# Performance work log

Measured on AMD Instinct MI355X. Metric: run time of the kernel, lower is better.

## Reference

```python
import jax, jax.numpy as jnp
import numpy as np

V, E, T, H, Z = 32000, 512, 64, 1024, 128
B = 64
PAD = 31999


def _lin(x, W, b):
    return x @ W.T + b


def _lstm_cell(x, h, c, Wih, Whh, bih, bhh):
    gates = x @ Wih.T + bih + h @ Whh.T + bhh  # [B,4H], torch gate order i,f,g,o
    i, f, g, o = jnp.split(gates, 4, axis=-1)
    c = jax.nn.sigmoid(f) * c + jax.nn.sigmoid(i) * jnp.tanh(g)
    h = jax.nn.sigmoid(o) * jnp.tanh(c)
    return h, c


def _forward(enc_input, dec_input, length, eps, enc_emb, enc_Wih, enc_Whh, enc_bih, enc_bhh,
             latent_W, latent_b, dec_emb, attn_W, attn_b, combine_W, combine_b,
             dec_Wih, dec_Whh, dec_bih, dec_bhh, pri_W, pri_b, inf_W, inf_b,
             aux_W, aux_b, out_W, out_b):
    # All lengths == T, so the descending sort and pack/pad are identity ops.
    att_mask = enc_input == PAD  # [B,T]
    x_enc = enc_emb[enc_input]   # [B,T,E]

    def enc_step(carry, x):
        h, c = carry
        h, c = _lstm_cell(x, h, c, enc_Wih, enc_Whh, enc_bih, enc_bhh)
        return (h, c), h

    h0 = jnp.zeros((B, H), x_enc.dtype)
    (h_T, c_T), enc_out = jax.lax.scan(enc_step, (h0, h0), jnp.swapaxes(x_enc, 0, 1))
    enc_output = jnp.swapaxes(enc_out, 0, 1)  # [B,T,H]

    mu, logvar = jnp.split(_lin(jnp.concatenate([h_T, c_T], -1), latent_W, latent_b), 2, -1)
    z = mu + jnp.exp(0.5 * logvar) * eps  # [B,Z]

    x_dec = dec_emb[dec_input]  # [B,T+1,E]; dropout off (eval mode)

    def dec_step(carry, inp):
        h, c = carry
        x, t = inp
        pri_mu, pri_lv = jnp.split(_lin(h, pri_W, pri_b), 2, -1)
        scale = _lin(jnp.concatenate([x, h], -1), attn_W, attn_b)  # [B,T]
        scale = jnp.where(att_mask, -jnp.inf, scale)
        attn_w = jax.nn.softmax(scale, -1)
        context = jnp.einsum('bt,bth->bh', attn_w, enc_output)
        inf_mu, inf_lv = jnp.split(_lin(jnp.concatenate([h, context], -1), inf_W, inf_b), 2, -1)
        mask = (length + 1 > t).astype(x.dtype)  # [B]
        kld = 0.5 * jnp.sum(pri_lv - inf_lv + jnp.exp(inf_lv - pri_lv)
                            + (inf_mu - pri_mu) ** 2 / jnp.exp(pri_lv) - 1.0, axis=1) * mask
        z_step = pri_mu  # eval mode (torch: reparameterize(inf_mu, inf_lv) when training)
        aux_mu = _lin(z_step, aux_W, aux_b)
        aux_c = jnp.sum((jax.lax.stop_gradient(context) - aux_mu) ** 2, axis=1)
        u = _lin(jnp.concatenate([x, aux_mu, z_step, z], -1), combine_W, combine_b)
        h, c = _lstm_cell(u, h, c, dec_Wih, dec_Whh, dec_bih, dec_bhh)
        return (h, c), (h, kld, aux_c)

    ts = jnp.arange(T + 1)
    _, (hs, klds, aux_cs) = jax.lax.scan(dec_step, (h0, h0), (jnp.swapaxes(x_dec, 0, 1), ts))
    output = jnp.swapaxes(hs, 0, 1)  # [B,T+1,H]

    logit = output @ out_W.T + out_b  # [B,T+1,V]
    logp = jax.nn.log_softmax(logit, -1)
    return logp, mu, logvar, jnp.sum(klds), jnp.sum(aux_cs)


def setup_inputs() -> dict:
    key = jax.random.key(0)
    ks = jax.random.split(key, 32)
    s = 0.02
    d = {
        'enc_input': jax.random.randint(ks[0], (B, T), 0, V - 1),
        'dec_input': jax.random.randint(ks[1], (B, T + 1), 0, V - 1),
        'length': jnp.full((B,), T, dtype=jnp.int32),
        'eps': jax.random.normal(ks[2], (B, Z), jnp.float32),
        'enc_emb': (jax.random.normal(ks[3], (V, E)) * s).at[PAD].set(0.0),
        'enc_Wih': jax.random.normal(ks[4], (4 * H, E)) * s,
        'enc_Whh': jax.random.normal(ks[5], (4 * H, H)) * s,
        'enc_bih': jax.random.normal(ks[6], (4 * H,)) * s,
        'enc_bhh': jax.random.normal(ks[7], (4 * H,)) * s,
        'latent_W': jax.random.normal(ks[8], (2 * Z, 2 * H)) * s,
        'latent_b': jax.random.normal(ks[9], (2 * Z,)) * s,
        'dec_emb': (jax.random.normal(ks[10], (V, E)) * s).at[PAD].set(0.0),
        'attn_W': jax.random.normal(ks[11], (T, H + E)) * s,
        'attn_b': jax.random.normal(ks[12], (T,)) * s,
        'combine_W': jax.random.normal(ks[13], (H, H + E + 2 * Z)) * s,
        'combine_b': jax.random.normal(ks[14], (H,)) * s,
        'dec_Wih': jax.random.normal(ks[15], (4 * H, H)) * s,
        'dec_Whh': jax.random.normal(ks[16], (4 * H, H)) * s,
        'dec_bih': jax.random.normal(ks[17], (4 * H,)) * s,
        'dec_bhh': jax.random.normal(ks[18], (4 * H,)) * s,
        'pri_W': jax.random.normal(ks[19], (2 * Z, H)) * s,
        'pri_b': jax.random.normal(ks[20], (2 * Z,)) * s,
        'inf_W': jax.random.normal(ks[21], (2 * Z, 2 * H)) * s,
        'inf_b': jax.random.normal(ks[22], (2 * Z,)) * s,
        'aux_W': jax.random.normal(ks[23], (H, Z)) * s,
        'aux_b': jax.random.normal(ks[24], (H,)) * s,
        'out_W': jax.random.normal(ks[25], (V, H)) * s,
        'out_b': jax.random.normal(ks[26], (V,)) * s,
    }
    return d


def reference(enc_input, dec_input, length, eps, enc_emb, enc_Wih, enc_Whh, enc_bih, enc_bhh,
              latent_W, latent_b, dec_emb, attn_W, attn_b, combine_W, combine_b,
              dec_Wih, dec_Whh, dec_bih, dec_bhh, pri_W, pri_b, inf_W, inf_b,
              aux_W, aux_b, out_W, out_b):
    return _forward(enc_input, dec_input, length, eps, enc_emb, enc_Wih, enc_Whh, enc_bih,
                    enc_bhh, latent_W, latent_b, dec_emb, attn_W, attn_b, combine_W, combine_b,
                    dec_Wih, dec_Whh, dec_bih, dec_bhh, pri_W, pri_b, inf_W, inf_b,
                    aux_W, aux_b, out_W, out_b)
```

## Files before the change

### kernel.cpp

```cpp
#include <hip/hip_runtime.h>
#include <hip/hip_bf16.h>
#include <cmath>

typedef unsigned short u16;
typedef __attribute__((ext_vector_type(8))) short short8;
typedef __attribute__((ext_vector_type(4))) float floatx4;

#define DEVI __device__ __forceinline__

constexpr int cV = 32000, cE = 512, cT = 64, cH = 1024, cZ = 128, cB = 64, cPAD = 31999, cTP1 = 65;
constexpr long long LOGP_SZ = 133120000LL;
constexpr long long AMAT_OFF = 130990080LL;
constexpr long long WBOUT_OFF = 38400000LL;
constexpr int SKIP_LO = 1200, SKIP_HI = 1712;

DEVI float b2f(u16 u) { return __uint_as_float(((unsigned)u) << 16); }
DEVI u16 f2b(float f) {
  unsigned u = __float_as_uint(f);
  unsigned r = u + 0x7FFFu + ((u >> 16) & 1u);
  return (u16)(r >> 16);
}
DEVI unsigned pk2(float lo, float hi) {
  __hip_bfloat162 t = __float22bfloat162_rn(make_float2(lo, hi));
  return *reinterpret_cast<unsigned*>(&t);
}
DEVI float sigm(float x) { return 1.f / (1.f + expf(-x)); }

DEVI short8 ldfragW(const float* __restrict__ p) {
  float4 x = *(const float4*)p, y = *(const float4*)(p + 4);
  union { unsigned u[4]; short8 s; } r;
  r.u[0] = pk2(x.x, x.y); r.u[1] = pk2(x.z, x.w);
  r.u[2] = pk2(y.x, y.y); r.u[3] = pk2(y.z, y.w);
  return r.s;
}

template <typename T>
DEVI short8 ldfrag(const T* __restrict__ p) {
  if constexpr (sizeof(T) == 2) return *(const short8*)(p);
  else return ldfragW((const float*)p);
}

template <int MAP>
DEVI int rmap(int r) {
  if constexpr (MAP == 1) return ((r & 3) << 10) | (r >> 2);
  else if constexpr (MAP == 2) return r & 63;
  else return r;
}

DEVI float dot_wf(const float* __restrict__ w, const float* __restrict__ s, int K) {
  float a0 = 0.f, a1 = 0.f, a2 = 0.f, a3 = 0.f;
#pragma unroll 4
  for (int k = 0; k < K; k += 8) {
    float4 p = *(const float4*)(w + k);
    float4 q = *(const float4*)(w + k + 4);
    a0 = fmaf(s[k + 0], p.x, a0); a1 = fmaf(s[k + 1], p.y, a1);
    a2 = fmaf(s[k + 2], p.z, a2); a3 = fmaf(s[k + 3], p.w, a3);
    a0 = fmaf(s[k + 4], q.x, a0); a1 = fmaf(s[k + 5], q.y, a1);
    a2 = fmaf(s[k + 6], q.z, a2); a3 = fmaf(s[k + 7], q.w, a3);
  }
  return (a0 + a1) + (a2 + a3);
}

__global__ __launch_bounds__(256) void k_zero(float* p, int n) {
  int i = blockIdx.x * 256 + threadIdx.x;
  if (i < n) p[i] = 0.f;
}

template <typename AT, typename BT, typename CT, int AMAP, int BMAP, bool ADDC>
__global__ __launch_bounds__(64) void k_gemm(
    const AT* __restrict__ A, int lda, const BT* __restrict__ B, int ldb,
    const float* __restrict__ bias, const float* __restrict__ Dm, int ldd,
    CT* __restrict__ C, int ldc, int K) {
  int nblk = blockIdx.x, mblk = blockIdx.y;
  int lane = threadIdx.x;
  int lr = lane & 15, kg = lane >> 4;
  const BT* Bp = B + (size_t)rmap<BMAP>(nblk * 16 + lr) * ldb + kg * 8;
  const AT* Ap[4];
#pragma unroll
  for (int mf = 0; mf < 4; mf++)
    Ap[mf] = A + (size_t)rmap<AMAP>(mblk * 64 + mf * 16 + lr) * lda + kg * 8;
  floatx4 acc[4];
#pragma unroll
  for (int mf = 0; mf < 4; mf++) acc[mf] = (floatx4){0.f, 0.f, 0.f, 0.f};
#pragma unroll 4
  for (int ks = 0; ks < K / 32; ks++) {
    short8 bv = ldfrag(Bp + ks * 32);
#pragma unroll
    for (int mf = 0; mf < 4; mf++) {
      short8 av = ldfrag(Ap[mf] + ks * 32);
      acc[mf] = __builtin_amdgcn_mfma_f32_16x16x32_bf16(av, bv, acc[mf], 0, 0, 0);
    }
  }
  int n = nblk * 16 + lr;
  float bs = bias ? bias[n] : 0.f;
#pragma unroll
  for (int mf = 0; mf < 4; mf++) {
#pragma unroll
    for (int jj = 0; jj < 4; jj++) {
      int m = mblk * 64 + mf * 16 + kg * 4 + jj;
      size_t ci = (size_t)m * ldc + n;
      float v = acc[mf][jj] + bs;
      if (Dm) v += Dm[(size_t)rmap<AMAP>(m) * ldd + n];
      if constexpr (ADDC) {
        if constexpr (sizeof(CT) == 2) v += b2f(C[ci]);
        else v += C[ci];
      }
      if constexpr (sizeof(CT) == 2) C[ci] = f2b(v);
      else C[ci] = v;
    }
  }
}

__global__ __launch_bounds__(64) void k_cell2(
    const u16* __restrict__ G, const u16* __restrict__ H, int strideH,
    const u16* __restrict__ Wb, float* __restrict__ c,
    u16* __restrict__ out1, int s1, u16* __restrict__ Afrag, int t) {
  int nb = blockIdx.x;
  int lane = threadIdx.x;
  int lr = lane & 15, kg = lane >> 4;
  const u16* Bp = Wb + (size_t)(nb * 16 + lr) * cH + kg * 8;
  floatx4 acc[4];
#pragma unroll
  for (int mf = 0; mf < 4; mf++) acc[mf] = (floatx4){0.f, 0.f, 0.f, 0.f};
#pragma unroll 8
  for (int ks = 0; ks < 32; ks++) {
    short8 bv = *(const short8*)(Bp + ks * 32);
#pragma unroll
    for (int mf = 0; mf < 4; mf++) {
      short8 av = *(const short8*)(H + (size_t)(mf * 16 + lr) * strideH + ks * 32 + kg * 8);
      acc[mf] = __builtin_amdgcn_mfma_f32_16x16x32_bf16(av, bv, acc[mf], 0, 0, 0);
    }
  }
  __shared__ float lds[16][65];
#pragma unroll
  for (int mf = 0; mf < 4; mf++)
#pragma unroll
    for (int jj = 0; jj < 4; jj++)
      lds[lr][mf * 16 + kg * 4 + jj] = acc[mf][jj];
  __syncthreads();
#pragma unroll
  for (int a = 0; a < 4; a++) {
    int b = lane;
    int j = nb * 4 + a;
    ushort4 gv = *(const ushort4*)(G + (size_t)b * 4096 + nb * 16 + 4 * a);
    float gi = lds[4 * a + 0][b] + b2f(gv.x);
    float gf = lds[4 * a + 1][b] + b2f(gv.y);
    float gg = lds[4 * a + 2][b] + b2f(gv.z);
    float go = lds[4 * a + 3][b] + b2f(gv.w);
    int ci = b * cH + j;
    float cc = c[ci];
    cc = sigm(gf) * cc + sigm(gi) * tanhf(gg);
    float hh = sigm(go) * tanhf(cc);
    c[ci] = cc;
    u16 hb = f2b(hh);
    out1[(size_t)b * s1 + j] = hb;
    if (Afrag) {
      int m = b * cTP1 + t;
      size_t idx = ((size_t)(m >> 4) * 32 + (j >> 5)) * 512 +
                   ((((j >> 3) & 3) * 16) + (m & 15)) * 8 + (j & 7);
      Afrag[idx] = hb;
    }
  }
}

__global__ __launch_bounds__(256) void k_tr(const float* __restrict__ src, int ld,
                                            int R, float* __restrict__ dst) {
  __shared__ float tile[32][33];
  int c0 = blockIdx.x * 32, r0 = blockIdx.y * 32;
  int tx = threadIdx.x & 31, ty = threadIdx.x >> 5;
  for (int i = ty; i < 32; i += 8) tile[i][tx] = src[(size_t)(r0 + i) * ld + c0 + tx];
  __syncthreads();
  for (int i = ty; i < 32; i += 8) dst[(size_t)(c0 + i) * R + r0 + tx] = tile[tx][i];
}

__global__ __launch_bounds__(256) void k_gemv(const float* __restrict__ W, int ld,
                                              const float* __restrict__ x,
                                              const float* __restrict__ b,
                                              float* __restrict__ out, int K, int add) {
  int n = blockIdx.x * 256 + threadIdx.x;
  const float* w = W + (size_t)n * ld;
  float s = b ? b[n] : 0.f;
  for (int k = 0; k < K; k += 4) {
    float4 wv = *(const float4*)(w + k);
    float4 xv = *(const float4*)(x + k);
    s += wv.x * xv.x + wv.y * xv.y + wv.z * xv.z + wv.w * xv.w;
  }
  if (add) out[n] += s; else out[n] = s;
}

__global__ __launch_bounds__(256) void k_biasD(const float* __restrict__ bih,
                                               const float* __restrict__ bhh,
                                               const float* __restrict__ Wih,
                                               const float* __restrict__ u0,
                                               float* __restrict__ biasD) {
  int np = blockIdx.x * 256 + threadIdx.x;
  int src = ((np & 3) << 10) | (np >> 2);
  const float* w = Wih + (size_t)src * cH;
  float s = bih[src] + bhh[src];
  for (int k = 0; k < cH; k += 4) {
    float4 wv = *(const float4*)(w + k);
    float4 xv = *(const float4*)(u0 + k);
    s += wv.x * xv.x + wv.y * xv.y + wv.z * xv.z + wv.w * xv.w;
  }
  biasD[np] = s;
}

__global__ __launch_bounds__(256) void k_biasE(const float* __restrict__ bih,
                                               const float* __restrict__ bhh,
                                               float* __restrict__ biasE) {
  int np = blockIdx.x * 256 + threadIdx.x;
  int src = ((np & 3) << 10) | (np >> 2);
  biasE[np] = bih[src] + bhh[src];
}

__global__ __launch_bounds__(256) void k_permW(const float* __restrict__ Whh,
                                               u16* __restrict__ Wp) {
  int np = blockIdx.x;
  int src = ((np & 3) << 10) | (np >> 2);
  const float* w = Whh + (size_t)src * cH;
  u16* d = Wp + (size_t)np * cH;
  int tid = threadIdx.x;
#pragma unroll
  for (int p = 0; p < 4; p++) d[tid + p * 256] = f2b(w[tid + p * 256]);
}

__global__ __launch_bounds__(256) void k_cvtW(const float* __restrict__ W,
                                              u16* __restrict__ Wf) {
  int g = blockIdx.x * 4 + (threadIdx.x >> 6);
  int l = threadIdx.x & 63;
  int nblk = g >> 5, kb = g & 31;
  const float* src = W + (size_t)(nblk * 16 + (l & 15)) * cH + kb * 32 + (l >> 4) * 8;
  *(short8*)(Wf + (size_t)g * 512 + l * 8) = ldfragW(src);
}

__global__ __launch_bounds__(256) void k_gather(const int* __restrict__ tok,
                                                const float* __restrict__ emb,
                                                u16* __restrict__ dst, int Tlen) {
  int r = blockIdx.x;
  int t = r >> 6, b = r & 63;
  const float* src = emb + (size_t)tok[b * Tlen + t] * cE;
  u16* d = dst + (size_t)r * cE;
  int tid = threadIdx.x;
  for (int k = tid; k < cE; k += 256) d[k] = f2b(src[k]);
}

__global__ __launch_bounds__(256) void k_latent(
    const u16* __restrict__ encO, const float* __restrict__ cT2,
    const float* __restrict__ W, const float* __restrict__ bias,
    float* __restrict__ mulv, float* __restrict__ outp) {
  __shared__ float s[2 * cH];
  int b = blockIdx.x;
  int n = threadIdx.x;
  for (int k = n; k < cH; k += 256) {
    s[k] = b2f(encO[((size_t)b * cT + 63) * cH + k]);
    s[cH + k] = cT2[b * cH + k];
  }
  __syncthreads();
  float acc = bias[n] + dot_wf(W + (size_t)n * (2 * cH), s, 2 * cH);
  mulv[b * 256 + n] = acc;
  if (n < cZ)
    outp[LOGP_SZ + (size_t)b * cZ + n] = acc;
  else
    outp[LOGP_SZ + (size_t)cB * cZ + (size_t)b * cZ + (n - cZ)] = acc;
}

__global__ __launch_bounds__(256) void k_z(const float* __restrict__ mulv,
                                           const float* __restrict__ eps,
                                           u16* __restrict__ zbuf) {
  int i = blockIdx.x * 256 + threadIdx.x;
  if (i >= cB * cZ) return;
  int b = i >> 7, zi = i & 127;
  float mu = mulv[b * 256 + zi], lv = mulv[b * 256 + cZ + zi];
  zbuf[i] = f2b(mu + expf(0.5f * lv) * eps[i]);
}

__global__ __launch_bounds__(256) void k_sctx(
    const float* __restrict__ S, const int* __restrict__ enc_input,
    const u16* __restrict__ encO, u16* __restrict__ ctxH) {
  __shared__ float wat[cT];
  int tb = blockIdx.x;
  int b = tb & 63;
  int tid = threadIdx.x;
  if (tid < cT) {
    float sc = S[(size_t)tb * cT + tid];
    if (enc_input[b * cT + tid] == cPAD) sc = -INFINITY;
    float m = sc;
#pragma unroll
    for (int off = 32; off >= 1; off >>= 1) m = fmaxf(m, __shfl_xor(m, off));
    float p = expf(sc - m);
    float ssum = p;
#pragma unroll
    for (int off = 32; off >= 1; off >>= 1) ssum += __shfl_xor(ssum, off);
    wat[tid] = p / ssum;
  }
  __syncthreads();
#pragma unroll
  for (int p = 0; p < 4; p++) {
    int j = tid + p * 256;
    float s = 0.f;
    const u16* e = encO + ((size_t)b * cT) * cH + j;
#pragma unroll 8
    for (int t2 = 0; t2 < cT; t2++) s += wat[t2] * b2f(e[(size_t)t2 * cH]);
    ctxH[(size_t)tb * cH + j] = f2b(s);
  }
}

__global__ __launch_bounds__(256) void k_scal_all(
    const float* __restrict__ priH, const float* __restrict__ infH,
    const u16* __restrict__ ctxH, const u16* __restrict__ auxH,
    const int* __restrict__ length, float* __restrict__ scal) {
  __shared__ float red[256];
  int tb = blockIdx.x;
  int t = tb >> 6, b = tb & 63;
  int tid = threadIdx.x;
  float r = 0.f;
  if (tid < cZ) {
    float pm = priH[(size_t)tb * 256 + tid], plv = priH[(size_t)tb * 256 + cZ + tid];
    float im = infH[(size_t)tb * 256 + tid], ilv = infH[(size_t)tb * 256 + cZ + tid];
    float d = im - pm;
    r = plv - ilv + expf(ilv - plv) + d * d * expf(-plv) - 1.f;
  }
  red[tid] = r;
  __syncthreads();
  for (int sft = 128; sft > 0; sft >>= 1) {
    if (tid < sft) red[tid] += red[tid + sft];
    __syncthreads();
  }
  if (tid == 0 && (length[b] + 1 > t)) atomicAdd(&scal[0], 0.5f * red[0]);
  __syncthreads();
  float r2 = 0.f;
#pragma unroll
  for (int p = 0; p < 4; p++) {
    int j = tid + p * 256;
    float d = b2f(ctxH[(size_t)tb * cH + j]) - b2f(auxH[(size_t)tb * cH + j]);
    r2 += d * d;
  }
  red[tid] = r2;
  __syncthreads();
  for (int sft = 128; sft > 0; sft >>= 1) {
    if (tid < sft) red[tid] += red[tid + sft];
    __syncthreads();
  }
  if (tid == 0) atomicAdd(&scal[1], red[0]);
}

__global__ void k_scal(const float* __restrict__ scal, float* __restrict__ outp) {
  if (threadIdx.x == 0) {
    outp[LOGP_SZ + 2 * cB * cZ] = scal[0];
    outp[LOGP_SZ + 2 * cB * cZ + 1] = scal[1];
  }
}

__global__ __launch_bounds__(256) void k_cpyA(const u16* __restrict__ src,
                                              u16* __restrict__ dst) {
  int i = blockIdx.x * 256 + threadIdx.x;
  ((uint4*)dst)[i] = ((const uint4*)(src + (size_t)252 * 32 * 512))[i];
}

template <bool WFRAG>
__global__ __launch_bounds__(512) void k_logit3(
    const u16* __restrict__ Af, int fragBase,
    const u16* __restrict__ Wf, const float* __restrict__ Wraw,
    const float* __restrict__ bias, float* __restrict__ outp,
    int mStart, int mEnd, int storeLo, int storeHi, int skipLo, int skipHi) {
  __shared__ u16 wpan[32768];
  int nb = blockIdx.x;
  int tid = threadIdx.x;
  if constexpr (WFRAG) {
    const uint4* src = (const uint4*)(Wf + (size_t)nb * 32768);
    uint4* dst = (uint4*)wpan;
#pragma unroll
    for (int q = 0; q < 8; q++) dst[tid + q * 512] = src[tid + q * 512];
  } else {
    int wv = tid >> 6, l = tid & 63;
    for (int f = wv; f < 64; f += 8) {
      int fr = f >> 5, kb = f & 31;
      const float* src = Wraw + (size_t)(nb * 32 + fr * 16 + (l & 15)) * cH + kb * 32 + (l >> 4) * 8;
      *(short8*)(wpan + f * 512 + l * 8) = ldfragW(src);
    }
  }
  __syncthreads();
  int wave = tid >> 6, lane = tid & 63;
  int lr = lane & 15, kg = lane >> 4;
  for (int m0 = mStart; m0 < mEnd; m0 += 512) {
    int mi = m0 + wave * 64;
    int mfg[4];
#pragma unroll
    for (int mf = 0; mf < 4; mf++) {
      int g = (mi >> 4) + mf;
      if (g > 259) g = 259;
      mfg[mf] = g - fragBase;
    }
    floatx4 acc[4][2];
#pragma unroll
    for (int mf = 0; mf < 4; mf++)
#pragma unroll
      for (int ni = 0; ni < 2; ni++) acc[mf][ni] = (floatx4){0.f, 0.f, 0.f, 0.f};
#pragma unroll 4
    for (int ks = 0; ks < 32; ks++) {
      short8 bv0 = *(const short8*)(wpan + ks * 512 + lane * 8);
      short8 bv1 = *(const short8*)(wpan + (32 + ks) * 512 + lane * 8);
#pragma unroll
      for (int mf = 0; mf < 4; mf++) {
        short8 av = *(const short8*)(Af + ((size_t)mfg[mf] * 32 + ks) * 512 + lane * 8);
        acc[mf][0] = __builtin_amdgcn_mfma_f32_16x16x32_bf16(av, bv0, acc[mf][0], 0, 0, 0);
        acc[mf][1] = __builtin_amdgcn_mfma_f32_16x16x32_bf16(av, bv1, acc[mf][1], 0, 0, 0);
      }
    }
#pragma unroll
    for (int mf = 0; mf < 4; mf++) {
#pragma unroll
      for (int ni = 0; ni < 2; ni++) {
        int n = nb * 32 + ni * 16 + lr;
        float bb = bias[n];
#pragma unroll
        for (int jj = 0; jj < 4; jj++) {
          int m = mi + mf * 16 + kg * 4 + jj;
          if (m >= storeLo && m < storeHi && !(m >= skipLo && m < skipHi))
            outp[(size_t)m * cV + n] = acc[mf][ni][jj] + bb;
        }
      }
    }
  }
}

__global__ __launch_bounds__(256) void k_lsm(float* __restrict__ outp) {
  __shared__ float wm_[4], ws_[4];
  __shared__ float blz;
  int m = blockIdx.x;
  int tid = threadIdx.x, lane = tid & 63, wid = tid >> 6;
  float4* rp4 = (float4*)(outp + (size_t)m * cV);
  float mx = -INFINITY, sm = 0.f;
  for (int n = tid; n < cV / 4; n += 256) {
    float4 v = rp4[n];
    float lm = fmaxf(fmaxf(v.x, v.y), fmaxf(v.z, v.w));
    float nm = fmaxf(mx, lm);
    sm = sm * expf(mx - nm) + expf(v.x - nm) + expf(v.y - nm) + expf(v.z - nm) + expf(v.w - nm);
    mx = nm;
  }
#pragma unroll
  for (int off = 32; off >= 1; off >>= 1) {
    float om = __shfl_xor(mx, off), os = __shfl_xor(sm, off);
    float nm = fmaxf(mx, om);
    sm = sm * expf(mx - nm) + os * expf(om - nm);
    mx = nm;
  }
  if (lane == 0) { wm_[wid] = mx; ws_[wid] = sm; }
  __syncthreads();
  if (tid == 0) {
    float M = fmaxf(fmaxf(wm_[0], wm_[1]), fmaxf(wm_[2], wm_[3]));
    float S = ws_[0] * expf(wm_[0] - M) + ws_[1] * expf(wm_[1] - M) +
              ws_[2] * expf(wm_[2] - M) + ws_[3] * expf(wm_[3] - M);
    blz = M + logf(S);
  }
  __syncthreads();
  float lz = blz;
  for (int n = tid; n < cV / 4; n += 256) {
    float4 v = rp4[n];
    v.x -= lz; v.y -= lz; v.z -= lz; v.w -= lz;
    rp4[n] = v;
  }
}

extern "C" void kernel_launch(void* const* d_in, const int* in_sizes, int n_in,
                              void* d_out, int out_size, void* d_ws, size_t ws_size,
                              hipStream_t stream) {
  (void)in_sizes; (void)n_in; (void)out_size; (void)ws_size;
  const int* enc_input  = (const int*)d_in[0];
  const int* dec_input  = (const int*)d_in[1];
  const int* length     = (const int*)d_in[2];
  const float* eps      = (const float*)d_in[3];
  const float* enc_emb  = (const float*)d_in[4];
  const float* enc_Wih  = (const float*)d_in[5];
  const float* enc_Whh  = (const float*)d_in[6];
  const float* enc_bih  = (const float*)d_in[7];
  const float* enc_bhh  = (const float*)d_in[8];
  const float* latent_W = (const float*)d_in[9];
  const float* latent_b = (const float*)d_in[10];
  const float* dec_emb  = (const float*)d_in[11];
  const float* attn_W   = (const float*)d_in[12];
  const float* attn_b   = (const float*)d_in[13];
  const float* comb_W   = (const float*)d_in[14];
  const float* comb_b   = (const float*)d_in[15];
  const float* dec_Wih  = (const float*)d_in[16];
  const float* dec_Whh  = (const float*)d_in[17];
  const float* dec_bih  = (const float*)d_in[18];
  const float* dec_bhh  = (const float*)d_in[19];
  const float* pri_W    = (const float*)d_in[20];
  const float* pri_b    = (const float*)d_in[21];
  const float* inf_W    = (const float*)d_in[22];
  const float* inf_b    = (const float*)d_in[23];
  const float* aux_W    = (const float*)d_in[24];
  const float* aux_b    = (const float*)d_in[25];
  const float* out_W    = (const float*)d_in[26];
  const float* out_b    = (const float*)d_in[27];
  float* outp = (float*)d_out;
  float* outF = outp;

  size_t off = 0;
  float* c_enc = outF + off; off += 65536;
  float* c_dec = outF + off; off += 65536;
  float* scal  = outF + off; off += 4;
  off += 60;
  u16* HencZ = (u16*)(outF + off); off += 32768;
  u16* Hh    = (u16*)(outF + off); off += 66 * 32768;
  size_t zeroSpan = 196672;
  u16* encO  = (u16*)(outF + off); off += 2097152;
  u16* Xenc  = (u16*)(outF + off); off += 1048576;
  u16* Xdec  = (u16*)(outF + off); off += 1064960;
  u16* zbuf  = (u16*)(outF + off); off += 4096;
  float* mulv  = outF + off; off += 16384;
  float* biasE = outF + off; off += 4096;
  float* biasD = outF + off; off += 4096;
  float* tmp1  = outF + off; off += 1024;
  float* u0    = outF + off; off += 1024;
  float* WcxT  = outF + off; off += 524288;
  float* WczT  = outF + off; off += 131072;
  float* wPmT  = outF + off; off += 131072;
  float* auxWT = outF + off; off += 131072;
  float* M1    = outF + off; off += 131072;
  float* WfT   = outF + off; off += 1048576;
  u16* WhhEp = (u16*)(outF + off); off += 2097152;
  u16* Wbig  = (u16*)(outF + off); off += 2097152;
  u16* C1    = (u16*)(outF + off); off += 1048576;
  u16* C2    = (u16*)(outF + off); off += 262144;
  u16* Genc  = (u16*)(outF + off); off += 8388608;
  u16* Gdec  = (u16*)(outF + off); off += 8519680;
  float* priH = outF + off; off += 1064960;
  float* infH = outF + off; off += 1064960;
  float* S    = outF + off; off += 266240;
  u16* ctxH  = (u16*)(outF + off); off += 2129920;
  u16* auxH  = (u16*)(outF + off); off += 2129920;
  u16* Wf   = (u16*)(outF + WBOUT_OFF);
  u16* Amat = (u16*)(outF + AMAT_OFF);
  u16* wsA = (u16*)d_ws;

  k_cvtW<<<16000, 256, 0, stream>>>(out_W, Wf);
  k_tr<<<dim3(16, 32), 256, 0, stream>>>(comb_W, 1792, 1024, WcxT);
  k_tr<<<dim3(4, 32), 256, 0, stream>>>(comb_W + 1664, 1792, 1024, WczT);
  k_tr<<<dim3(32, 4), 256, 0, stream>>>(pri_W, 1024, 128, wPmT);
  k_tr<<<dim3(4, 32), 256, 0, stream>>>(aux_W, 128, 1024, auxWT);
  k_gemv<<<4, 256, 0, stream>>>(aux_W, 128, pri_b, aux_b, tmp1, 128, 0);
  k_gemv<<<4, 256, 0, stream>>>(comb_W + 512, 1792, tmp1, comb_b, u0, 1024, 0);
  k_gemv<<<4, 256, 0, stream>>>(comb_W + 1536, 1792, pri_b, nullptr, u0, 128, 1);
  k_biasE<<<16, 256, 0, stream>>>(enc_bih, enc_bhh, biasE);
  k_biasD<<<16, 256, 0, stream>>>(dec_bih, dec_bhh, dec_Wih, u0, biasD);
  k_permW<<<4096, 256, 0, stream>>>(enc_Whh, WhhEp);
  k_gather<<<cT * cB, 256, 0, stream>>>(enc_input, enc_emb, Xenc, cT);
  k_gather<<<cTP1 * cB, 256, 0, stream>>>(dec_input, dec_emb, Xdec, cTP1);
  k_zero<<<(int)((zeroSpan + 255) / 256), 256, 0, stream>>>(c_enc, (int)zeroSpan);

  k_gemm<float, float, float, 0, 0, false><<<dim3(8, 16), 64, 0, stream>>>(
      comb_W + 512, 1792, auxWT, 1024, nullptr, comb_W + 1536, 1792, M1, 128, 1024);
  k_gemm<float, float, float, 0, 0, false><<<dim3(64, 16), 64, 0, stream>>>(
      wPmT, 128, M1, 128, nullptr, nullptr, 0, WfT, 1024, 128);
  k_gemm<float, float, u16, 1, 0, false><<<dim3(64, 64), 64, 0, stream>>>(
      dec_Wih, 1024, WfT, 1024, nullptr, dec_Whh, 1024, Wbig, 1024, 1024);
  k_gemm<float, float, u16, 1, 0, false><<<dim3(32, 64), 64, 0, stream>>>(
      dec_Wih, 1024, WcxT, 1024, nullptr, nullptr, 0, C1, 512, 1024);
  k_gemm<float, float, u16, 1, 0, false><<<dim3(8, 64), 64, 0, stream>>>(
      dec_Wih, 1024, WczT, 1024, nullptr, nullptr, 0, C2, 128, 1024);
  k_gemm<u16, float, u16, 0, 1, false><<<dim3(256, 64), 64, 0, stream>>>(
      Xenc, 512, enc_Wih, 512, biasE, nullptr, 0, Genc, 4096, 512);

  for (int t = 0; t < cT; t++) {
    const u16* Hcur = t ? (encO + (size_t)(t - 1) * cH) : HencZ;
    int sH = t ? (cT * cH) : cH;
    k_cell2<<<256, 64, 0, stream>>>(Genc + (size_t)t * cB * 4096, Hcur, sH, WhhEp,
                                    c_enc, encO + (size_t)t * cH, cT * cH, nullptr, 0);
  }
  k_latent<<<cB, 256, 0, stream>>>(encO, c_enc, latent_W, latent_b, mulv, outp);
  k_z<<<(cB * cZ + 255) / 256, 256, 0, stream>>>(mulv, eps, zbuf);

  k_gemm<u16, u16, u16, 0, 0, false><<<dim3(256, 65), 64, 0, stream>>>(
      Xdec, 512, C1, 512, biasD, nullptr, 0, Gdec, 4096, 512);
  k_gemm<u16, u16, u16, 2, 0, true><<<dim3(256, 65), 64, 0, stream>>>(
      zbuf, 128, C2, 128, nullptr, nullptr, 0, Gdec, 4096, 128);

  for (int t = 0; t < cTP1; t++) {
    k_cell2<<<256, 64, 0, stream>>>(Gdec + (size_t)t * cB * 4096,
                                    Hh + (size_t)t * cB * cH, cH, Wbig, c_dec,
                                    Hh + (size_t)(t + 1) * cB * cH, cH,
                                    Amat, t);
  }

  k_gemm<u16, float, float, 0, 0, false><<<dim3(16, 65), 64, 0, stream>>>(
      Hh, 1024, pri_W, 1024, pri_b, nullptr, 0, priH, 256, 1024);
  k_gemm<u16, float, float, 0, 0, false><<<dim3(4, 65), 64, 0, stream>>>(
      Xdec, 512, attn_W, 1536, attn_b, nullptr, 0, S, 64, 512);
  k_gemm<u16, float, float, 0, 0, true><<<dim3(4, 65), 64, 0, stream>>>(
      Hh, 1024, attn_W + 512, 1536, nullptr, nullptr, 0, S, 64, 1024);
  k_sctx<<<cTP1 * cB, 256, 0, stream>>>(S, enc_input, encO, ctxH);
  k_gemm<u16, float, float, 0, 0, false><<<dim3(16, 65), 64, 0, stream>>>(
      Hh, 1024, inf_W, 2048, inf_b, nullptr, 0, infH, 256, 1024);
  k_gemm<u16, float, float, 0, 0, true><<<dim3(16, 65), 64, 0, stream>>>(
      ctxH, 1024, inf_W + 1024, 2048, nullptr, nullptr, 0, infH, 256, 1024);
  k_gemm<float, float, u16, 0, 0, false><<<dim3(64, 65), 64, 0, stream>>>(
      priH, 256, aux_W, 128, aux_b, nullptr, 0, auxH, 1024, 128);
  k_scal_all<<<cTP1 * cB, 256, 0, stream>>>(priH, infH, ctxH, auxH, length, scal);
  k_scal<<<1, 64, 0, stream>>>(scal, outp);

  k_cpyA<<<32, 256, 0, stream>>>(Amat, wsA);
  k_logit3<true><<<1000, 512, 0, stream>>>(Amat, 0, Wf, nullptr, out_b, outp,
                                           0, 4096, 0, 4093, SKIP_LO, SKIP_HI);
  k_logit3<false><<<1000, 512, 0, stream>>>(Amat, 0, nullptr, out_W, out_b, outp,
                                            SKIP_LO, SKIP_HI, SKIP_LO, SKIP_HI, 0, 0);
  k_logit3<false><<<1000, 512, 0, stream>>>(wsA, 252, nullptr, out_W, out_b, outp,
                                            4032, 4160, 4093, 4160, 0, 0);
  k_lsm<<<cB * cTP1, 256, 0, stream>>>(outp);
}
```

Before: 4.017 ms.

## Use fragment-packed weights and hidden state in LSTM steps, widen logit tiles

Pre-packs the encoder/decoder recurrent weights and input-projection weights into MFMA fragment order, so the GEMMs and the per-step cell kernel load contiguous short8 fragments instead of strided rows. The cell kernel now ping-pongs a fragment-layout hidden state and writes its outputs with vectorized ushort4/float4 stores. The logit kernel moves from 32 to 64 vocab columns per block with K split into two halves staged through the same LDS panel, halving the block count and reusing each A fragment across four B tiles. This adds workspace buffers and extra sync points in the logit kernel, and it relies on the shifted skip/offset constants staying consistent.

```diff
diff --git a/kernel.cpp b/kernel.cpp
--- a/kernel.cpp
+++ b/kernel.cpp
@@ -11,8 +11,8 @@
 constexpr int cV = 32000, cE = 512, cT = 64, cH = 1024, cZ = 128, cB = 64, cPAD = 31999, cTP1 = 65;
 constexpr long long LOGP_SZ = 133120000LL;
 constexpr long long AMAT_OFF = 130990080LL;
-constexpr long long WBOUT_OFF = 38400000LL;
-constexpr int SKIP_LO = 1200, SKIP_HI = 1712;
+constexpr long long WBOUT_OFF = 39936000LL;
+constexpr int SKIP_LO = 1248, SKIP_HI = 1760;
 
 DEVI float b2f(u16 u) { return __uint_as_float(((unsigned)u) << 16); }
 DEVI u16 f2b(float f) {
@@ -66,7 +66,8 @@
   if (i < n) p[i] = 0.f;
 }
 
-template <typename AT, typename BT, typename CT, int AMAP, int BMAP, bool ADDC>
+template <typename AT, typename BT, typename CT, int AMAP, int BMAP, bool ADDC,
+          int BFRAGKB = 0, bool CFRAG = false>
 __global__ __launch_bounds__(64) void k_gemm(
     const AT* __restrict__ A, int lda, const BT* __restrict__ B, int ldb,
     const float* __restrict__ bias, const float* __restrict__ Dm, int ldd,
@@ -84,7 +85,11 @@
   for (int mf = 0; mf < 4; mf++) acc[mf] = (floatx4){0.f, 0.f, 0.f, 0.f};
 #pragma unroll 4
   for (int ks = 0; ks < K / 32; ks++) {
-    short8 bv = ldfrag(Bp + ks * 32);
+    short8 bv;
+    if constexpr (BFRAGKB > 0)
+      bv = *(const short8*)((const u16*)B + ((size_t)nblk * BFRAGKB + ks) * 512 + lane * 8);
+    else
+      bv = ldfrag(Bp + ks * 32);
 #pragma unroll
     for (int mf = 0; mf < 4; mf++) {
       short8 av = ldfrag(Ap[mf] + ks * 32);
@@ -98,36 +103,45 @@
 #pragma unroll
     for (int jj = 0; jj < 4; jj++) {
       int m = mblk * 64 + mf * 16 + kg * 4 + jj;
-      size_t ci = (size_t)m * ldc + n;
       float v = acc[mf][jj] + bs;
       if (Dm) v += Dm[(size_t)rmap<AMAP>(m) * ldd + n];
-      if constexpr (ADDC) {
-        if constexpr (sizeof(CT) == 2) v += b2f(C[ci]);
-        else v += C[ci];
+      if constexpr (CFRAG) {
+        size_t fi = ((size_t)(m >> 4) * (ldc >> 5) + (n >> 5)) * 512 +
+                    (size_t)((((n >> 3) & 3) * 16 + (m & 15)) * 8 + (n & 7));
+        ((u16*)C)[fi] = f2b(v);
+      } else {
+        size_t ci = (size_t)m * ldc + n;
+        if constexpr (ADDC) {
+          if constexpr (sizeof(CT) == 2) v += b2f(C[ci]);
+          else v += C[ci];
+        }
+        if constexpr (sizeof(CT) == 2) C[ci] = f2b(v);
+        else C[ci] = v;
       }
-      if constexpr (sizeof(CT) == 2) C[ci] = f2b(v);
-      else C[ci] = v;
     }
   }
 }
 
-__global__ __launch_bounds__(64) void k_cell2(
-    const u16* __restrict__ G, const u16* __restrict__ H, int strideH,
-    const u16* __restrict__ Wb, float* __restrict__ c,
-    u16* __restrict__ out1, int s1, u16* __restrict__ Afrag, int t) {
+__global__ __launch_bounds__(64) void k_cell3(
+    const u16* __restrict__ G,
+    const u16* __restrict__ Hf,
+    const u16* __restrict__ Wbf,
+    float* __restrict__ c,
+    u16* __restrict__ outRM, int s1,
+    u16* __restrict__ HfOut,
+    u16* __restrict__ Afrag, int t) {
   int nb = blockIdx.x;
   int lane = threadIdx.x;
   int lr = lane & 15, kg = lane >> 4;
-  const u16* Bp = Wb + (size_t)(nb * 16 + lr) * cH + kg * 8;
   floatx4 acc[4];
 #pragma unroll
   for (int mf = 0; mf < 4; mf++) acc[mf] = (floatx4){0.f, 0.f, 0.f, 0.f};
 #pragma unroll 8
   for (int ks = 0; ks < 32; ks++) {
-    short8 bv = *(const short8*)(Bp + ks * 32);
+    short8 bv = *(const short8*)(Wbf + ((size_t)nb * 32 + ks) * 512 + lane * 8);
 #pragma unroll
     for (int mf = 0; mf < 4; mf++) {
-      short8 av = *(const short8*)(H + (size_t)(mf * 16 + lr) * strideH + ks * 32 + kg * 8);
+      short8 av = *(const short8*)(Hf + ((size_t)mf * 32 + ks) * 512 + lane * 8);
       acc[mf] = __builtin_amdgcn_mfma_f32_16x16x32_bf16(av, bv, acc[mf], 0, 0, 0);
     }
   }
@@ -138,28 +152,36 @@
     for (int jj = 0; jj < 4; jj++)
       lds[lr][mf * 16 + kg * 4 + jj] = acc[mf][jj];
   __syncthreads();
+  int b = lane;
+  const u16* gp = G + (size_t)b * 4096 + nb * 16;
+  float4 cc4 = *(const float4*)(c + (size_t)b * cH + nb * 4);
+  float cin[4] = {cc4.x, cc4.y, cc4.z, cc4.w};
+  float ncc[4];
+  u16 hb[4];
 #pragma unroll
   for (int a = 0; a < 4; a++) {
-    int b = lane;
-    int j = nb * 4 + a;
-    ushort4 gv = *(const ushort4*)(G + (size_t)b * 4096 + nb * 16 + 4 * a);
-    float gi = lds[4 * a + 0][b] + b2f(gv.x);
-    float gf = lds[4 * a + 1][b] + b2f(gv.y);
-    float gg = lds[4 * a + 2][b] + b2f(gv.z);
-    float go = lds[4 * a + 3][b] + b2f(gv.w);
-    int ci = b * cH + j;
-    float cc = c[ci];
+    float gi = lds[4 * a + 0][b] + b2f(gp[4 * a + 0]);
+    float gf = lds[4 * a + 1][b] + b2f(gp[4 * a + 1]);
+    float gg = lds[4 * a + 2][b] + b2f(gp[4 * a + 2]);
+    float go = lds[4 * a + 3][b] + b2f(gp[4 * a + 3]);
+    float cc = cin[a];
     cc = sigm(gf) * cc + sigm(gi) * tanhf(gg);
     float hh = sigm(go) * tanhf(cc);
-    c[ci] = cc;
-    u16 hb = f2b(hh);
-    out1[(size_t)b * s1 + j] = hb;
-    if (Afrag) {
-      int m = b * cTP1 + t;
-      size_t idx = ((size_t)(m >> 4) * 32 + (j >> 5)) * 512 +
-                   ((((j >> 3) & 3) * 16) + (m & 15)) * 8 + (j & 7);
-      Afrag[idx] = hb;
-    }
+    ncc[a] = cc;
+    hb[a] = f2b(hh);
+  }
+  *(float4*)(c + (size_t)b * cH + nb * 4) = make_float4(ncc[0], ncc[1], ncc[2], ncc[3]);
+  ushort4 hv = {hb[0], hb[1], hb[2], hb[3]};
+  *(ushort4*)(outRM + (size_t)b * s1 + nb * 4) = hv;
+  int j0 = nb * 4;
+  size_t hidx = ((size_t)(b >> 4) * 32 + (j0 >> 5)) * 512 +
+                (size_t)((((j0 >> 3) & 3) * 16 + (b & 15)) * 8 + (j0 & 7));
+  *(ushort4*)(HfOut + hidx) = hv;
+  if (Afrag) {
+    int m = b * cTP1 + t;
+    size_t aidx = ((size_t)(m >> 4) * 32 + (j0 >> 5)) * 512 +
+                  (size_t)((((j0 >> 3) & 3) * 16 + (m & 15)) * 8 + (j0 & 7));
+    *(ushort4*)(Afrag + aidx) = hv;
   }
 }
 
@@ -213,15 +235,16 @@
   biasE[np] = bih[src] + bhh[src];
 }
 
-__global__ __launch_bounds__(256) void k_permW(const float* __restrict__ Whh,
-                                               u16* __restrict__ Wp) {
-  int np = blockIdx.x;
+__global__ __launch_bounds__(256) void k_packP(const float* __restrict__ W,
+                                               u16* __restrict__ Wf, int K) {
+  int g = blockIdx.x * 4 + (threadIdx.x >> 6);
+  int l = threadIdx.x & 63;
+  int KB = K >> 5;
+  int nblk = g / KB, kb = g % KB;
+  int np = nblk * 16 + (l & 15);
   int src = ((np & 3) << 10) | (np >> 2);
-  const float* w = Whh + (size_t)src * cH;
-  u16* d = Wp + (size_t)np * cH;
-  int tid = threadIdx.x;
-#pragma unroll
-  for (int p = 0; p < 4; p++) d[tid + p * 256] = f2b(w[tid + p * 256]);
+  const float* s = W + (size_t)src * K + kb * 32 + (l >> 4) * 8;
+  *(short8*)(Wf + (size_t)g * 512 + l * 8) = ldfragW(s);
 }
 
 __global__ __launch_bounds__(256) void k_cvtW(const float* __restrict__ W,
@@ -358,7 +381,7 @@
 }
 
 template <bool WFRAG>
-__global__ __launch_bounds__(512) void k_logit3(
+__global__ __launch_bounds__(512) void k_logit4(
     const u16* __restrict__ Af, int fragBase,
     const u16* __restrict__ Wf, const float* __restrict__ Wraw,
     const float* __restrict__ bias, float* __restrict__ outp,
@@ -366,20 +389,6 @@
   __shared__ u16 wpan[32768];
   int nb = blockIdx.x;
   int tid = threadIdx.x;
-  if constexpr (WFRAG) {
-    const uint4* src = (const uint4*)(Wf + (size_t)nb * 32768);
-    uint4* dst = (uint4*)wpan;
-#pragma unroll
-    for (int q = 0; q < 8; q++) dst[tid + q * 512] = src[tid + q * 512];
-  } else {
-    int wv = tid >> 6, l = tid & 63;
-    for (int f = wv; f < 64; f += 8) {
-      int fr = f >> 5, kb = f & 31;
-      const float* src = Wraw + (size_t)(nb * 32 + fr * 16 + (l & 15)) * cH + kb * 32 + (l >> 4) * 8;
-      *(short8*)(wpan + f * 512 + l * 8) = ldfragW(src);
-    }
-  }
-  __syncthreads();
   int wave = tid >> 6, lane = tid & 63;
   int lr = lane & 15, kg = lane >> 4;
   for (int m0 = mStart; m0 < mEnd; m0 += 512) {
@@ -391,33 +400,57 @@
       if (g > 259) g = 259;
       mfg[mf] = g - fragBase;
     }
-    floatx4 acc[4][2];
+    floatx4 acc[4][4];
 #pragma unroll
     for (int mf = 0; mf < 4; mf++)
 #pragma unroll
-      for (int ni = 0; ni < 2; ni++) acc[mf][ni] = (floatx4){0.f, 0.f, 0.f, 0.f};
+      for (int fr = 0; fr < 4; fr++) acc[mf][fr] = (floatx4){0.f, 0.f, 0.f, 0.f};
+    for (int h = 0; h < 2; h++) {
+      __syncthreads();
+      if constexpr (WFRAG) {
+#pragma unroll
+        for (int q = 0; q < 8; q++) {
+          int idx = q * 4096 + tid * 8;
+          int lf = idx >> 9, wi = idx & 511;
+          int fr = lf >> 4, kbl = lf & 15;
+          size_t g = (size_t)(nb * 4 + fr) * 32 + h * 16 + kbl;
+          *(uint4*)(wpan + idx) = *(const uint4*)(Wf + g * 512 + wi);
+        }
+      } else {
+        for (int f = wave; f < 64; f += 8) {
+          int fr = f >> 4, kbl = f & 15;
+          const float* src = Wraw + (size_t)(nb * 64 + fr * 16 + lr) * cH +
+                             h * 512 + kbl * 32 + kg * 8;
+          *(short8*)(wpan + (size_t)f * 512 + lane * 8) = ldfragW(src);
+        }
+      }
+      __syncthreads();
 #pragma unroll 4
-    for (int ks = 0; ks < 32; ks++) {
-      short8 bv0 = *(const short8*)(wpan + ks * 512 + lane * 8);
-      short8 bv1 = *(const short8*)(wpan + (32 + ks) * 512 + lane * 8);
-#pragma unroll
-      for (int mf = 0; mf < 4; mf++) {
-        short8 av = *(const short8*)(Af + ((size_t)mfg[mf] * 32 + ks) * 512 + lane * 8);
-        acc[mf][0] = __builtin_amdgcn_mfma_f32_16x16x32_bf16(av, bv0, acc[mf][0], 0, 0, 0);
-        acc[mf][1] = __builtin_amdgcn_mfma_f32_16x16x32_bf16(av, bv1, acc[mf][1], 0, 0, 0);
+      for (int ks = 0; ks < 16; ks++) {
+        short8 bv[4];
+#pragma unroll
+        for (int fr = 0; fr < 4; fr++)
+          bv[fr] = *(const short8*)(wpan + ((size_t)(fr * 16 + ks) * 512) + lane * 8);
+#pragma unroll
+        for (int mf = 0; mf < 4; mf++) {
+          short8 av = *(const short8*)(Af + ((size_t)mfg[mf] * 32 + h * 16 + ks) * 512 + lane * 8);
+#pragma unroll
+          for (int fr = 0; fr < 4; fr++)
+            acc[mf][fr] = __builtin_amdgcn_mfma_f32_16x16x32_bf16(av, bv[fr], acc[mf][fr], 0, 0, 0);
+        }
       }
     }
 #pragma unroll
     for (int mf = 0; mf < 4; mf++) {
 #pragma unroll
-      for (int ni = 0; ni < 2; ni++) {
-        int n = nb * 32 + ni * 16 + lr;
+      for (int fr = 0; fr < 4; fr++) {
+        int n = nb * 64 + fr * 16 + lr;
         float bb = bias[n];
 #pragma unroll
         for (int jj = 0; jj < 4; jj++) {
           int m = mi + mf * 16 + kg * 4 + jj;
           if (m >= storeLo && m < storeHi && !(m >= skipLo && m < skipHi))
-            outp[(size_t)m * cV + n] = acc[mf][ni][jj] + bb;
+            outp[(size_t)m * cV + n] = acc[mf][fr][jj] + bb;
         }
       }
     }
@@ -502,9 +535,12 @@
   float* c_dec = outF + off; off += 65536;
   float* scal  = outF + off; off += 4;
   off += 60;
-  u16* HencZ = (u16*)(outF + off); off += 32768;
-  u16* Hh    = (u16*)(outF + off); off += 66 * 32768;
-  size_t zeroSpan = 196672;
+  u16* HfEncA = (u16*)(outF + off); off += 32768;
+  u16* HfDecA = (u16*)(outF + off); off += 32768;
+  u16* Hh     = (u16*)(outF + off); off += 66 * 32768;
+  size_t zeroSpan = 229440;
+  u16* HfEncB = (u16*)(outF + off); off += 32768;
+  u16* HfDecB = (u16*)(outF + off); off += 32768;
   u16* encO  = (u16*)(outF + off); off += 2097152;
   u16* Xenc  = (u16*)(outF + off); off += 1048576;
   u16* Xdec  = (u16*)(outF + off); off += 1064960;
@@ -520,10 +556,11 @@
   float* auxWT = outF + off; off += 131072;
   float* M1    = outF + off; off += 131072;
   float* WfT   = outF + off; off += 1048576;
-  u16* WhhEp = (u16*)(outF + off); off += 2097152;
-  u16* Wbig  = (u16*)(outF + off); off += 2097152;
-  u16* C1    = (u16*)(outF + off); off += 1048576;
-  u16* C2    = (u16*)(outF + off); off += 262144;
+  u16* WhhEpF = (u16*)(outF + off); off += 2097152;
+  u16* WbigF  = (u16*)(outF + off); off += 2097152;
+  u16* C1f    = (u16*)(outF + off); off += 1048576;
+  u16* C2f    = (u16*)(outF + off); off += 262144;
+  u16* WihEf  = (u16*)(outF + off); off += 1048576;
   u16* Genc  = (u16*)(outF + off); off += 8388608;
   u16* Gdec  = (u16*)(outF + off); off += 8519680;
   float* priH = outF + off; off += 1064960;
@@ -545,7 +582,8 @@
   k_gemv<<<4, 256, 0, stream>>>(comb_W + 1536, 1792, pri_b, nullptr, u0, 128, 1);
   k_biasE<<<16, 256, 0, stream>>>(enc_bih, enc_bhh, biasE);
   k_biasD<<<16, 256, 0, stream>>>(dec_bih, dec_bhh, dec_Wih, u0, biasD);
-  k_permW<<<4096, 256, 0, stream>>>(enc_Whh, WhhEp);
+  k_packP<<<2048, 256, 0, stream>>>(enc_Whh, WhhEpF, 1024);
+  k_packP<<<1024, 256, 0, stream>>>(enc_Wih, WihEf, 512);
   k_gather<<<cT * cB, 256, 0, stream>>>(enc_input, enc_emb, Xenc, cT);
   k_gather<<<cTP1 * cB, 256, 0, stream>>>(dec_input, dec_emb, Xdec, cTP1);
   k_zero<<<(int)((zeroSpan + 255) / 256), 256, 0, stream>>>(c_enc, (int)zeroSpan);
@@ -554,34 +592,36 @@
       comb_W + 512, 1792, auxWT, 1024, nullptr, comb_W + 1536, 1792, M1, 128, 1024);
   k_gemm<float, float, float, 0, 0, false><<<dim3(64, 16), 64, 0, stream>>>(
       wPmT, 128, M1, 128, nullptr, nullptr, 0, WfT, 1024, 128);
-  k_gemm<float, float, u16, 1, 0, false><<<dim3(64, 64), 64, 0, stream>>>(
-      dec_Wih, 1024, WfT, 1024, nullptr, dec_Whh, 1024, Wbig, 1024, 1024);
-  k_gemm<float, float, u16, 1, 0, false><<<dim3(32, 64), 64, 0, stream>>>(
-      dec_Wih, 1024, WcxT, 1024, nullptr, nullptr, 0, C1, 512, 1024);
-  k_gemm<float, float, u16, 1, 0, false><<<dim3(8, 64), 64, 0, stream>>>(
-      dec_Wih, 1024, WczT, 1024, nullptr, nullptr, 0, C2, 128, 1024);
-  k_gemm<u16, float, u16, 0, 1, false><<<dim3(256, 64), 64, 0, stream>>>(
-      Xenc, 512, enc_Wih, 512, biasE, nullptr, 0, Genc, 4096, 512);
+  k_gemm<float, float, u16, 1, 0, false, 0, true><<<dim3(64, 64), 64, 0, stream>>>(
+      dec_Wih, 1024, WfT, 1024, nullptr, dec_Whh, 1024, WbigF, 1024, 1024);
+  k_gemm<float, float, u16, 1, 0, false, 0, true><<<dim3(32, 64), 64, 0, stream>>>(
+      dec_Wih, 1024, WcxT, 1024, nullptr, nullptr, 0, C1f, 512, 1024);
+  k_gemm<float, float, u16, 1, 0, false, 0, true><<<dim3(8, 64), 64, 0, stream>>>(
+      dec_Wih, 1024, WczT, 1024, nullptr, nullptr, 0, C2f, 128, 1024);
+  k_gemm<u16, u16, u16, 0, 0, false, 16, false><<<dim3(256, 64), 64, 0, stream>>>(
+      Xenc, 512, WihEf, 512, biasE, nullptr, 0, Genc, 4096, 512);
 
   for (int t = 0; t < cT; t++) {
-    const u16* Hcur = t ? (encO + (size_t)(t - 1) * cH) : HencZ;
-    int sH = t ? (cT * cH) : cH;
-    k_cell2<<<256, 64, 0, stream>>>(Genc + (size_t)t * cB * 4096, Hcur, sH, WhhEp,
-                                    c_enc, encO + (size_t)t * cH, cT * cH, nullptr, 0);
+    const u16* hin = (t & 1) ? HfEncB : HfEncA;
+    u16* hout = (t & 1) ? HfEncA : HfEncB;
+    k_cell3<<<256, 64, 0, stream>>>(Genc + (size_t)t * cB * 4096, hin, WhhEpF,
+                                    c_enc, encO + (size_t)t * cH, cT * cH,
+                                    hout, nullptr, 0);
   }
   k_latent<<<cB, 256, 0, stream>>>(encO, c_enc, latent_W, latent_b, mulv, outp);
   k_z<<<(cB * cZ + 255) / 256, 256, 0, stream>>>(mulv, eps, zbuf);
 
-  k_gemm<u16, u16, u16, 0, 0, false><<<dim3(256, 65), 64, 0, stream>>>(
-      Xdec, 512, C1, 512, biasD, nullptr, 0, Gdec, 4096, 512);
-  k_gemm<u16, u16, u16, 2, 0, true><<<dim3(256, 65), 64, 0, stream>>>(
-      zbuf, 128, C2, 128, nullptr, nullptr, 0, Gdec, 4096, 128);
+  k_gemm<u16, u16, u16, 0, 0, false, 16, false><<<dim3(256, 65), 64, 0, stream>>>(
+      Xdec, 512, C1f, 512, biasD, nullptr, 0, Gdec, 4096, 512);
+  k_gemm<u16, u16, u16, 2, 0, true, 4, false><<<dim3(256, 65), 64, 0, stream>>>(
+      zbuf, 128, C2f, 128, nullptr, nullptr, 0, Gdec, 4096, 128);
 
   for (int t = 0; t < cTP1; t++) {
-    k_cell2<<<256, 64, 0, stream>>>(Gdec + (size_t)t * cB * 4096,
-                                    Hh + (size_t)t * cB * cH, cH, Wbig, c_dec,
-                                    Hh + (size_t)(t + 1) * cB * cH, cH,
-                                    Amat, t);
+    const u16* hin = (t & 1) ? HfDecB : HfDecA;
+    u16* hout = (t & 1) ? HfDecA : HfDecB;
+    k_cell3<<<256, 64, 0, stream>>>(Gdec + (size_t)t * cB * 4096, hin, WbigF,
+                                    c_dec, Hh + (size_t)(t + 1) * cB * cH, cH,
+                                    hout, Amat, t);
   }
 
   k_gemm<u16, float, float, 0, 0, false><<<dim3(16, 65), 64, 0, stream>>>(
@@ -601,11 +641,11 @@
   k_scal<<<1, 64, 0, stream>>>(scal, outp);
 
   k_cpyA<<<32, 256, 0, stream>>>(Amat, wsA);
-  k_logit3<true><<<1000, 512, 0, stream>>>(Amat, 0, Wf, nullptr, out_b, outp,
-                                           0, 4096, 0, 4093, SKIP_LO, SKIP_HI);
-  k_logit3<false><<<1000, 512, 0, stream>>>(Amat, 0, nullptr, out_W, out_b, outp,
-                                            SKIP_LO, SKIP_HI, SKIP_LO, SKIP_HI, 0, 0);
-  k_logit3<false><<<1000, 512, 0, stream>>>(wsA, 252, nullptr, out_W, out_b, outp,
-                                            4032, 4160, 4093, 4160, 0, 0);
+  k_logit4<true><<<500, 512, 0, stream>>>(Amat, 0, Wf, nullptr, out_b, outp,
+                                          0, 4096, 0, 4093, SKIP_LO, SKIP_HI);
+  k_logit4<false><<<500, 512, 0, stream>>>(Amat, 0, nullptr, out_W, out_b, outp,
+                                           SKIP_LO, SKIP_HI, SKIP_LO, SKIP_HI, 0, 0);
+  k_logit4<false><<<500, 512, 0, stream>>>(wsA, 252, nullptr, out_W, out_b, outp,
+                                           4032, 4160, 4093, 4160, 0, 0);
   k_lsm<<<cB * cTP1, 256, 0, stream>>>(outp);
 }
```

Result: slower. 5.107 ms (+27.1%).
